# Kernel tuning notes

Hardware: AMD Instinct MI355X
Metric: run time of the kernel (lower is better)

Reference implementation:

```python
import jax, jax.numpy as jnp
import numpy as np

B, T, D_IN, EMB, H = 2, 2048, 1024, 1024, 16
HD = EMB // H  # head_dim = 64


def setup_inputs() -> dict:
    key = jax.random.key(0)
    ks = jax.random.split(key, 3)
    scale_qkv = 1.0 / np.sqrt(D_IN)
    scale_o = 1.0 / np.sqrt(EMB)
    return {
        "x": jax.random.normal(ks[0], (B, T, D_IN), dtype=jnp.float32),
        "W_qkv": jax.random.normal(ks[1], (D_IN, 3 * EMB), dtype=jnp.float32) * scale_qkv,
        "b_qkv": jnp.zeros((3 * EMB,), dtype=jnp.float32),
        "W_o": jax.random.normal(ks[2], (EMB, EMB), dtype=jnp.float32) * scale_o,
        "b_o": jnp.zeros((EMB,), dtype=jnp.float32),
    }


def reference(x, W_qkv, b_qkv, W_o, b_o):
    b, t, _ = x.shape
    qkv = x @ W_qkv + b_qkv                      # [B,T,3*EMB]
    # Match torch: reshape to (B,T,H,3*HD) -> permute -> chunk into q,k,v
    qkv = qkv.reshape(b, t, H, 3 * HD).transpose(0, 2, 1, 3)  # [B,H,T,3*HD]
    q, k, v = jnp.split(qkv, 3, axis=-1)         # each [B,H,T,HD]
    scale = 1.0 / jnp.sqrt(jnp.asarray(HD, dtype=q.dtype))
    scores = jnp.einsum("bhqd,bhkd->bhqk", q, k) * scale  # [B,H,T,T]
    attn = jax.nn.softmax(scores, axis=-1)
    values = jnp.einsum("bhqk,bhkd->bhqd", attn, v)       # [B,H,T,HD]
    values = values.transpose(0, 2, 1, 3).reshape(b, t, EMB)
    return values @ W_o + b_o
```

## Files before the change

kernel.cpp:

```cpp
#include <hip/hip_runtime.h>
#include <math.h>

typedef __bf16 bf16x8 __attribute__((ext_vector_type(8)));
typedef float f32x4 __attribute__((ext_vector_type(4)));

#define GPTR(p) ((const __attribute__((address_space(1))) void*)(p))
#define LPTR(p) ((__attribute__((address_space(3))) void*)(p))

#define QSCALE 0.18033688011112042f

__device__ __forceinline__ unsigned short f2bf(float f) {
  unsigned int u = __float_as_uint(f);
  u += 0x7FFFu + ((u >> 16) & 1u);
  return (unsigned short)(u >> 16);
}

__device__ __forceinline__ unsigned int pack_bf2(float lo, float hi) {
  return __builtin_amdgcn_perm(__float_as_uint(hi) + 0x8000u,
                               __float_as_uint(lo) + 0x8000u, 0x07060302u);
}

__device__ __forceinline__ float fast_exp2(float x) {
#if __has_builtin(__builtin_amdgcn_exp2f)
  return __builtin_amdgcn_exp2f(x);
#else
  return exp2f(x);
#endif
}

__device__ __forceinline__ f32x4 zero4() {
  f32x4 z; z[0] = 0.f; z[1] = 0.f; z[2] = 0.f; z[3] = 0.f; return z;
}

__device__ __forceinline__ void permlane_swap32(unsigned int& a, unsigned int& b) {
  asm("v_permlane32_swap_b32 %0, %1" : "+v"(a), "+v"(b));
}
__device__ __forceinline__ void permlane_swap16(unsigned int& a, unsigned int& b) {
  asm("v_permlane16_swap_b32 %0, %1" : "+v"(a), "+v"(b));
}

__global__ void prep(const float* __restrict__ x, unsigned short* __restrict__ xb,
                     const float* __restrict__ Wqkv, unsigned short* __restrict__ wqkvt,
                     const float* __restrict__ Wo, unsigned short* __restrict__ wot) {
  __shared__ float tile[64][65];
  const int bid = blockIdx.x, t = threadIdx.x;
  if (bid < 4096) {
    int i = (bid * 256 + t) * 4;
    float4 v = *(const float4*)(x + i);
    ushort4 o;
    o.x = f2bf(v.x); o.y = f2bf(v.y); o.z = f2bf(v.z); o.w = f2bf(v.w);
    *(ushort4*)(xb + i) = o;
    return;
  }
  const float* in; unsigned short* out; int K, N, bx, by;
  if (bid < 4096 + 768) {
    int id = bid - 4096; bx = id % 48; by = id / 48;
    in = Wqkv; out = wqkvt; K = 1024; N = 3072;
  } else {
    int id = bid - 4864; bx = id % 16; by = id / 16;
    in = Wo; out = wot; K = 1024; N = 1024;
  }
  int k0 = by * 64, n0 = bx * 64;
#pragma unroll
  for (int p = 0; p < 16; ++p) {
    int l = p * 256 + t; int r = l >> 6, c = l & 63;
    tile[r][c] = in[(size_t)(k0 + r) * N + n0 + c];
  }
  __syncthreads();
#pragma unroll
  for (int p = 0; p < 16; ++p) {
    int l = p * 256 + t; int r = l >> 6, c = l & 63;
    out[(size_t)(n0 + r) * K + k0 + c] = f2bf(tile[c][r]);
  }
}

__global__ __launch_bounds__(256) void gemm_qkv(
    const unsigned short* __restrict__ A, const unsigned short* __restrict__ Bt,
    const float* __restrict__ bias,
    unsigned short* __restrict__ Qd, unsigned short* __restrict__ Kd,
    unsigned short* __restrict__ Vtd) {
  __shared__ unsigned short As[2][4096];
  __shared__ unsigned short Bs[2][4096];
  const int tid = threadIdx.x, wave = tid >> 6, lane = tid & 63;
  const int quad = lane >> 4, l16 = lane & 15;
  const int wm = (wave >> 1) * 64, wn = (wave & 1) * 64;
  const int flat = blockIdx.y * 24 + blockIdx.x;
  const int nf = (flat & 7) * 96 + (flat >> 3);
  const int m0 = (nf / 24) * 128, n0 = (nf % 24) * 128;
  f32x4 acc[4][4];
#pragma unroll
  for (int i = 0; i < 4; ++i)
#pragma unroll
    for (int j = 0; j < 4; ++j) acc[i][j] = zero4();

  const int c = wave * 64 + lane;
  const int rA = c >> 2, o16 = (c & 3) * 8;

#define STAGEQ(B, K0)                                                                      \
  do {                                                                                     \
    __builtin_amdgcn_global_load_lds(GPTR(A + (size_t)(m0 + rA) * 1024 + (K0) + o16),      \
                                     LPTR(&As[B][wave * 512]), 16, 0, 0);                  \
    __builtin_amdgcn_global_load_lds(GPTR(A + (size_t)(m0 + 64 + rA) * 1024 + (K0) + o16), \
                                     LPTR(&As[B][2048 + wave * 512]), 16, 0, 0);           \
    __builtin_amdgcn_global_load_lds(GPTR(Bt + (size_t)(n0 + rA) * 1024 + (K0) + o16),     \
                                     LPTR(&Bs[B][wave * 512]), 16, 0, 0);                  \
    __builtin_amdgcn_global_load_lds(GPTR(Bt + (size_t)(n0 + 64 + rA) * 1024 + (K0) + o16),\
                                     LPTR(&Bs[B][2048 + wave * 512]), 16, 0, 0);           \
  } while (0)

  STAGEQ(0, 0);
  __syncthreads();
  int cur = 0;
  for (int k0 = 0; k0 < 1024; k0 += 32) {
    if (k0 < 992) STAGEQ(cur ^ 1, k0 + 32);
    bf16x8 af[4], bfr[4];
#pragma unroll
    for (int mt = 0; mt < 4; ++mt)
      af[mt] = *(const bf16x8*)(&As[cur][(wm + mt * 16 + l16) * 32 + quad * 8]);
#pragma unroll
    for (int nt = 0; nt < 4; ++nt)
      bfr[nt] = *(const bf16x8*)(&Bs[cur][(wn + nt * 16 + l16) * 32 + quad * 8]);
#pragma unroll
    for (int mt = 0; mt < 4; ++mt)
#pragma unroll
      for (int nt = 0; nt < 4; ++nt)
        acc[mt][nt] = __builtin_amdgcn_mfma_f32_16x16x32_bf16(af[mt], bfr[nt], acc[mt][nt], 0, 0, 0);
    __syncthreads();
    cur ^= 1;
  }
#undef STAGEQ

#pragma unroll
  for (int mt = 0; mt < 4; ++mt) {
#pragma unroll
    for (int nt = 0; nt < 4; ++nt) {
      int m = m0 + wm + mt * 16 + quad * 4;
      int n = n0 + wn + nt * 16 + l16;
      float bv = bias[n];
      int h = n / 192, rem = n - h * 192;
      int which = rem >> 6, d = rem & 63;
      int b = m >> 11, t0 = m & 2047;
      size_t head = (size_t)(b * 16 + h);
      f32x4 a = acc[mt][nt];
      if (which == 0) {
        size_t base = (head * 2048 + t0) * 64 + d;
#pragma unroll
        for (int i = 0; i < 4; ++i)
          Qd[base + (size_t)i * 64] = f2bf((a[i] + bv) * QSCALE);
      } else if (which == 1) {
        size_t base = head * 131072 + (size_t)(t0 >> 6) * 4096;
#pragma unroll
        for (int i = 0; i < 4; ++i) {
          int tt = t0 + i;
          Kd[base + (tt & 63) * 64 + (((d >> 3) ^ (tt & 7)) << 3) + (d & 7)] = f2bf(a[i] + bv);
        }
      } else {
        size_t base = head * 131072 + (size_t)(t0 >> 6) * 4096;
        ushort4 o;
        o.x = f2bf(a[0] + bv); o.y = f2bf(a[1] + bv);
        o.z = f2bf(a[2] + bv); o.w = f2bf(a[3] + bv);
        *(ushort4*)(Vtd + base + d * 64 + (((((t0 & 63) >> 3)) ^ (d & 7)) << 3) + (t0 & 7)) = o;
      }
    }
  }
}

__global__ __launch_bounds__(256, 2) void flash_attn(
    const unsigned short* __restrict__ Qg,
    const unsigned short* __restrict__ Kg,
    const unsigned short* __restrict__ Vg,
    unsigned short* __restrict__ att) {
  __shared__ unsigned short SM[16384];
  __shared__ float Lbuf[2][64];
  const int tid = threadIdx.x, wave = tid >> 6, lane = tid & 63;
  const int quad = lane >> 4, l16 = lane & 15;
  const int h7 = l16 & 7;
  const int wq = wave >> 1, wk = wave & 1;
  const int flat = blockIdx.y * 16 + blockIdx.x;
  const int nf = (flat & 7) * 64 + (flat >> 3);
  const int bh = nf >> 4;
  const int q0 = (nf & 15) * 128 + wq * 64;

  bf16x8 bq[4][2];
#pragma unroll
  for (int qg = 0; qg < 4; ++qg)
#pragma unroll
    for (int kh = 0; kh < 2; ++kh)
      bq[qg][kh] = *(const bf16x8*)(Qg + ((size_t)bh * 2048 + q0 + qg * 16 + l16) * 64 + kh * 32 + quad * 8);

  union { unsigned short u[8]; bf16x8 v; } onesu;
#pragma unroll
  for (int i = 0; i < 8; ++i) onesu.u[i] = 0x3F80;
  const bf16x8 ones = onesu.v;

  f32x4 o[4][4], l_acc[4];
#pragma unroll
  for (int qg = 0; qg < 4; ++qg) {
    l_acc[qg] = zero4();
#pragma unroll
    for (int i = 0; i < 4; ++i) o[qg][i] = zero4();
  }

  const unsigned short* Kt = Kg + (size_t)bh * 131072 + lane * 8;
  const unsigned short* Vt = Vg + (size_t)bh * 131072 + lane * 8;
  unsigned short* KsB = SM;
  unsigned short* VsB = SM + 8192;
  const int so0 = wave * 512, so1 = (4 + wave) * 512;

#define STAGE_KV(buf, tile)                                                              \
  do {                                                                                   \
    const unsigned short* Kb_ = Kt + (tile) * 4096;                                      \
    const unsigned short* Vb_ = Vt + (tile) * 4096;                                      \
    __builtin_amdgcn_global_load_lds(GPTR(Kb_ + so0), LPTR(KsB + (buf) * 4096 + so0), 16, 0, 0); \
    __builtin_amdgcn_global_load_lds(GPTR(Kb_ + so1), LPTR(KsB + (buf) * 4096 + so1), 16, 0, 0); \
    __builtin_amdgcn_global_load_lds(GPTR(Vb_ + so0), LPTR(VsB + (buf) * 4096 + so0), 16, 0, 0); \
    __builtin_amdgcn_global_load_lds(GPTR(Vb_ + so1), LPTR(VsB + (buf) * 4096 + so1), 16, 0, 0); \
  } while (0)

  STAGE_KV(0, 0);
  __syncthreads();

  int cur = 0;
  for (int tile = 0; tile < 32; ++tile) {
    if (tile < 31) STAGE_KV(cur ^ 1, tile + 1);
    const unsigned short* Kc = KsB + cur * 4096;
    const unsigned short* Vc = VsB + cur * 4096;

    f32x4 s[4][2];
#pragma unroll
    for (int qg = 0; qg < 4; ++qg) { s[qg][0] = zero4(); s[qg][1] = zero4(); }
#pragma unroll
    for (int kt = 0; kt < 2; ++kt) {
#pragma unroll
      for (int kh = 0; kh < 2; ++kh) {
        bf16x8 a = *(const bf16x8*)(Kc + (wk * 32 + kt * 16 + l16) * 64 + (((kh * 4 + quad) ^ h7) << 3));
#pragma unroll
        for (int qg = 0; qg < 4; ++qg)
          s[qg][kt] = __builtin_amdgcn_mfma_f32_16x16x32_bf16(a, bq[qg][kh], s[qg][kt], 0, 0, 0);
      }
    }

    unsigned int pw[4][2][2];
#pragma unroll
    for (int qg = 0; qg < 4; ++qg) {
#pragma unroll
      for (int kt = 0; kt < 2; ++kt) {
        float p0 = fast_exp2(s[qg][kt][0]);
        float p1 = fast_exp2(s[qg][kt][1]);
        float p2 = fast_exp2(s[qg][kt][2]);
        float p3 = fast_exp2(s[qg][kt][3]);
        pw[qg][kt][0] = pack_bf2(p0, p1);
        pw[qg][kt][1] = pack_bf2(p2, p3);
      }
    }

    bf16x8 pf[4];
#pragma unroll
    for (int qg = 0; qg < 4; ++qg) {
      unsigned int a0 = pw[qg][0][0], b0 = pw[qg][1][0];
      unsigned int a1 = pw[qg][0][1], b1 = pw[qg][1][1];
      permlane_swap32(a0, b0); permlane_swap16(a0, b0);
      permlane_swap32(a1, b1); permlane_swap16(a1, b1);
      union { unsigned int u[4]; bf16x8 v; } x;
      x.u[0] = a0; x.u[1] = a1; x.u[2] = b0; x.u[3] = b1;
      pf[qg] = x.v;
    }

#pragma unroll
    for (int qg = 0; qg < 4; ++qg)
      l_acc[qg] = __builtin_amdgcn_mfma_f32_16x16x32_bf16(ones, pf[qg], l_acc[qg], 0, 0, 0);

#pragma unroll
    for (int mt = 0; mt < 4; ++mt) {
      bf16x8 av = *(const bf16x8*)(Vc + (mt * 16 + l16) * 64 + (((wk * 4 + quad) ^ h7) << 3));
#pragma unroll
      for (int qg = 0; qg < 4; ++qg)
        o[qg][mt] = __builtin_amdgcn_mfma_f32_16x16x32_bf16(av, pf[qg], o[qg][mt], 0, 0, 0);
    }

    __syncthreads();
    cur ^= 1;
  }
#undef STAGE_KV

  float* Obuf = (float*)SM;
  if (wk == 1) {
#pragma unroll
    for (int qg = 0; qg < 4; ++qg) {
#pragma unroll
      for (int mt = 0; mt < 4; ++mt) {
        int cc = (mt * 4 + quad) ^ l16;
        *(f32x4*)(Obuf + wq * 4096 + (qg * 16 + l16) * 64 + cc * 4) = o[qg][mt];
      }
      if (quad == 0) Lbuf[wq][qg * 16 + l16] = l_acc[qg][0];
    }
  }
  __syncthreads();
  if (wk == 0) {
    int b = bh >> 4, h = bh & 15;
#pragma unroll
    for (int qg = 0; qg < 4; ++qg) {
      float inv_l = 1.f / (l_acc[qg][0] + Lbuf[wq][qg * 16 + l16]);
      unsigned short* orow = att + ((size_t)b * 2048 + q0 + qg * 16 + l16) * 1024 + h * 64;
#pragma unroll
      for (int mt = 0; mt < 4; ++mt) {
        int cc = (mt * 4 + quad) ^ l16;
        f32x4 other = *(const f32x4*)(Obuf + wq * 4096 + (qg * 16 + l16) * 64 + cc * 4);
        ushort4 ov;
        ov.x = f2bf((o[qg][mt][0] + other[0]) * inv_l);
        ov.y = f2bf((o[qg][mt][1] + other[1]) * inv_l);
        ov.z = f2bf((o[qg][mt][2] + other[2]) * inv_l);
        ov.w = f2bf((o[qg][mt][3] + other[3]) * inv_l);
        *(ushort4*)(orow + mt * 16 + quad * 4) = ov;
      }
    }
  }
}

__global__ __launch_bounds__(256) void gemm_out(
    const unsigned short* __restrict__ A, const unsigned short* __restrict__ Bt,
    const float* __restrict__ bias, float* __restrict__ out) {
  __shared__ unsigned short As[2][4096];
  __shared__ unsigned short Bs[2][2048];
  const int tid = threadIdx.x, wave = tid >> 6, lane = tid & 63;
  const int quad = lane >> 4, l16 = lane & 15;
  const int wm = (wave >> 1) * 64, wn = (wave & 1) * 32;
  const int flat = blockIdx.y * 16 + blockIdx.x;
  const int nf = (flat & 7) * 64 + (flat >> 3);
  const int m0 = (nf >> 4) * 128, n0 = (nf & 15) * 64;
  f32x4 acc[4][2];
#pragma unroll
  for (int i = 0; i < 4; ++i)
#pragma unroll
    for (int j = 0; j < 2; ++j) acc[i][j] = zero4();

  const int c = wave * 64 + lane;
  const int rA = c >> 2, o16 = (c & 3) * 8;

#define STAGEO(B, K0)                                                                      \
  do {                                                                                     \
    __builtin_amdgcn_global_load_lds(GPTR(A + (size_t)(m0 + rA) * 1024 + (K0) + o16),      \
                                     LPTR(&As[B][wave * 512]), 16, 0, 0);                  \
    __builtin_amdgcn_global_load_lds(GPTR(A + (size_t)(m0 + 64 + rA) * 1024 + (K0) + o16), \
                                     LPTR(&As[B][2048 + wave * 512]), 16, 0, 0);           \
    __builtin_amdgcn_global_load_lds(GPTR(Bt + (size_t)(n0 + rA) * 1024 + (K0) + o16),     \
                                     LPTR(&Bs[B][wave * 512]), 16, 0, 0);                  \
  } while (0)

  STAGEO(0, 0);
  __syncthreads();
  int cur = 0;
  for (int k0 = 0; k0 < 1024; k0 += 32) {
    if (k0 < 992) STAGEO(cur ^ 1, k0 + 32);
    bf16x8 af[4], bfr[2];
#pragma unroll
    for (int mt = 0; mt < 4; ++mt)
      af[mt] = *(const bf16x8*)(&As[cur][(wm + mt * 16 + l16) * 32 + quad * 8]);
#pragma unroll
    for (int nt = 0; nt < 2; ++nt)
      bfr[nt] = *(const bf16x8*)(&Bs[cur][(wn + nt * 16 + l16) * 32 + quad * 8]);
#pragma unroll
    for (int mt = 0; mt < 4; ++mt)
#pragma unroll
      for (int nt = 0; nt < 2; ++nt)
        acc[mt][nt] = __builtin_amdgcn_mfma_f32_16x16x32_bf16(af[mt], bfr[nt], acc[mt][nt], 0, 0, 0);
    __syncthreads();
    cur ^= 1;
  }
#undef STAGEO

#pragma unroll
  for (int mt = 0; mt < 4; ++mt) {
#pragma unroll
    for (int nt = 0; nt < 2; ++nt) {
      int m = m0 + wm + mt * 16 + quad * 4;
      int n = n0 + wn + nt * 16 + l16;
      float bv = bias[n];
      float* orow = out + (size_t)m * 1024 + n;
      orow[0]        = acc[mt][nt][0] + bv;
      orow[1024]     = acc[mt][nt][1] + bv;
      orow[2 * 1024] = acc[mt][nt][2] + bv;
      orow[3 * 1024] = acc[mt][nt][3] + bv;
    }
  }
}

extern "C" void kernel_launch(void* const* d_in, const int* in_sizes, int n_in,
                              void* d_out, int out_size, void* d_ws, size_t ws_size,
                              hipStream_t stream) {
  const float* x    = (const float*)d_in[0];
  const float* Wqkv = (const float*)d_in[1];
  const float* bqkv = (const float*)d_in[2];
  const float* Wo   = (const float*)d_in[3];
  const float* bo   = (const float*)d_in[4];
  float* out = (float*)d_out;

  unsigned short* xb    = (unsigned short*)d_ws;
  unsigned short* wqkvt = xb    + (size_t)4096 * 1024;
  unsigned short* wot   = wqkvt + (size_t)3072 * 1024;
  unsigned short* Qd    = wot   + (size_t)1024 * 1024;
  unsigned short* Kd    = Qd    + (size_t)32 * 2048 * 64;
  unsigned short* Vtd   = Kd    + (size_t)32 * 2048 * 64;
  unsigned short* attb  = Vtd   + (size_t)32 * 2048 * 64;

  prep<<<4096 + 768 + 256, 256, 0, stream>>>(x, xb, Wqkv, wqkvt, Wo, wot);
  gemm_qkv<<<dim3(24, 32), 256, 0, stream>>>(xb, wqkvt, bqkv, Qd, Kd, Vtd);
  flash_attn<<<dim3(16, 32), 256, 0, stream>>>(Qd, Kd, Vtd, attb);
  gemm_out<<<dim3(16, 32), 256, 0, stream>>>(attb, wot, bo, out);
}
```

Before: 190.0 us.

## Split attention KV range in two with atomic fp32 partials and combine kernel

```diff
diff --git a/kernel.cpp b/kernel.cpp
--- a/kernel.cpp
+++ b/kernel.cpp
@@ -39,9 +39,8 @@
   asm("v_permlane16_swap_b32 %0, %1" : "+v"(a), "+v"(b));
 }
 
-__global__ void prep(const float* __restrict__ x, unsigned short* __restrict__ xb,
-                     const float* __restrict__ Wqkv, unsigned short* __restrict__ wqkvt,
-                     const float* __restrict__ Wo, unsigned short* __restrict__ wot) {
+__global__ void prep_a(const float* __restrict__ x, unsigned short* __restrict__ xb,
+                       const float* __restrict__ Wqkv, unsigned short* __restrict__ wqkvt) {
   __shared__ float tile[64][65];
   const int bid = blockIdx.x, t = threadIdx.x;
   if (bid < 4096) {
@@ -52,15 +51,28 @@
     *(ushort4*)(xb + i) = o;
     return;
   }
-  const float* in; unsigned short* out; int K, N, bx, by;
-  if (bid < 4096 + 768) {
-    int id = bid - 4096; bx = id % 48; by = id / 48;
-    in = Wqkv; out = wqkvt; K = 1024; N = 3072;
-  } else {
-    int id = bid - 4864; bx = id % 16; by = id / 16;
-    in = Wo; out = wot; K = 1024; N = 1024;
-  }
+  int id = bid - 4096;
+  int bx = id % 48, by = id / 48;
+  const int K = 1024, N = 3072;
   int k0 = by * 64, n0 = bx * 64;
+#pragma unroll
+  for (int p = 0; p < 16; ++p) {
+    int l = p * 256 + t; int r = l >> 6, c = l & 63;
+    tile[r][c] = Wqkv[(size_t)(k0 + r) * N + n0 + c];
+  }
+  __syncthreads();
+#pragma unroll
+  for (int p = 0; p < 16; ++p) {
+    int l = p * 256 + t; int r = l >> 6, c = l & 63;
+    wqkvt[(size_t)(n0 + r) * K + k0 + c] = f2bf(tile[c][r]);
+  }
+}
+
+__global__ void transpose_conv(const float* __restrict__ in, unsigned short* __restrict__ out,
+                               int K, int N) {
+  __shared__ float tile[64][65];
+  int k0 = blockIdx.y * 64, n0 = blockIdx.x * 64;
+  int t = threadIdx.x;
 #pragma unroll
   for (int p = 0; p < 16; ++p) {
     int l = p * 256 + t; int r = l >> 6, c = l & 63;
@@ -169,7 +181,8 @@
     const unsigned short* __restrict__ Qg,
     const unsigned short* __restrict__ Kg,
     const unsigned short* __restrict__ Vg,
-    unsigned short* __restrict__ att) {
+    float* __restrict__ Po,
+    float* __restrict__ Pl) {
   __shared__ unsigned short SM[16384];
   __shared__ float Lbuf[2][64];
   const int tid = threadIdx.x, wave = tid >> 6, lane = tid & 63;
@@ -177,9 +190,12 @@
   const int h7 = l16 & 7;
   const int wq = wave >> 1, wk = wave & 1;
   const int flat = blockIdx.y * 16 + blockIdx.x;
-  const int nf = (flat & 7) * 64 + (flat >> 3);
-  const int bh = nf >> 4;
-  const int q0 = (nf & 15) * 128 + wq * 64;
+  const int nf = (flat & 7) * 128 + (flat >> 3);
+  const int bh = nf >> 5;
+  const int half = (nf >> 4) & 1;
+  const int qb = nf & 15;
+  const int q0 = qb * 128 + wq * 64;
+  const int tbase = half * 16;
 
   bf16x8 bq[4][2];
 #pragma unroll
@@ -217,12 +233,12 @@
     __builtin_amdgcn_global_load_lds(GPTR(Vb_ + so1), LPTR(VsB + (buf) * 4096 + so1), 16, 0, 0); \
   } while (0)
 
-  STAGE_KV(0, 0);
+  STAGE_KV(0, tbase);
   __syncthreads();
 
   int cur = 0;
-  for (int tile = 0; tile < 32; ++tile) {
-    if (tile < 31) STAGE_KV(cur ^ 1, tile + 1);
+  for (int it = 0; it < 16; ++it) {
+    if (it < 15) STAGE_KV(cur ^ 1, tbase + it + 1);
     const unsigned short* Kc = KsB + cur * 4096;
     const unsigned short* Vc = VsB + cur * 4096;
 
@@ -297,24 +313,40 @@
   }
   __syncthreads();
   if (wk == 0) {
-    int b = bh >> 4, h = bh & 15;
 #pragma unroll
     for (int qg = 0; qg < 4; ++qg) {
-      float inv_l = 1.f / (l_acc[qg][0] + Lbuf[wq][qg * 16 + l16]);
-      unsigned short* orow = att + ((size_t)b * 2048 + q0 + qg * 16 + l16) * 1024 + h * 64;
+      size_t prow = (size_t)bh * 2048 + q0 + qg * 16 + l16;
+      float* po = Po + prow * 64;
+      float lsum = l_acc[qg][0] + Lbuf[wq][qg * 16 + l16];
 #pragma unroll
       for (int mt = 0; mt < 4; ++mt) {
         int cc = (mt * 4 + quad) ^ l16;
         f32x4 other = *(const f32x4*)(Obuf + wq * 4096 + (qg * 16 + l16) * 64 + cc * 4);
-        ushort4 ov;
-        ov.x = f2bf((o[qg][mt][0] + other[0]) * inv_l);
-        ov.y = f2bf((o[qg][mt][1] + other[1]) * inv_l);
-        ov.z = f2bf((o[qg][mt][2] + other[2]) * inv_l);
-        ov.w = f2bf((o[qg][mt][3] + other[3]) * inv_l);
-        *(ushort4*)(orow + mt * 16 + quad * 4) = ov;
+#pragma unroll
+        for (int i = 0; i < 4; ++i)
+          atomicAdd(po + mt * 16 + quad * 4 + i, o[qg][mt][i] + other[i]);
       }
-    }
-  }
+      if (quad == 0) atomicAdd(Pl + prow, lsum);
+    }
+  }
+}
+
+__global__ __launch_bounds__(256) void combine_attn(
+    const float* __restrict__ Po, const float* __restrict__ Pl,
+    unsigned short* __restrict__ att) {
+  int g = blockIdx.x * 256 + threadIdx.x;
+  int row = g >> 4;
+  int dq = (g & 15) * 4;
+  int bh = row >> 11, q = row & 2047;
+  float inv = 1.f / Pl[row];
+  float4 a = *(const float4*)(Po + (size_t)row * 64 + dq);
+  ushort4 o;
+  o.x = f2bf(a.x * inv);
+  o.y = f2bf(a.y * inv);
+  o.z = f2bf(a.z * inv);
+  o.w = f2bf(a.w * inv);
+  int b_ = bh >> 4, h = bh & 15;
+  *(ushort4*)(att + ((size_t)(b_ * 2048 + q)) * 1024 + h * 64 + dq) = o;
 }
 
 __global__ __launch_bounds__(256) void gemm_out(
@@ -398,13 +430,19 @@
   unsigned short* xb    = (unsigned short*)d_ws;
   unsigned short* wqkvt = xb    + (size_t)4096 * 1024;
   unsigned short* wot   = wqkvt + (size_t)3072 * 1024;
+  float*          Po    = (float*)d_ws;
   unsigned short* Qd    = wot   + (size_t)1024 * 1024;
   unsigned short* Kd    = Qd    + (size_t)32 * 2048 * 64;
   unsigned short* Vtd   = Kd    + (size_t)32 * 2048 * 64;
   unsigned short* attb  = Vtd   + (size_t)32 * 2048 * 64;
-
-  prep<<<4096 + 768 + 256, 256, 0, stream>>>(x, xb, Wqkv, wqkvt, Wo, wot);
+  float*          Pl    = out;
+
+  prep_a<<<4096 + 768, 256, 0, stream>>>(x, xb, Wqkv, wqkvt);
   gemm_qkv<<<dim3(24, 32), 256, 0, stream>>>(xb, wqkvt, bqkv, Qd, Kd, Vtd);
-  flash_attn<<<dim3(16, 32), 256, 0, stream>>>(Qd, Kd, Vtd, attb);
+  hipMemsetAsync(Po, 0, (size_t)65536 * 64 * sizeof(float), stream);
+  hipMemsetAsync(Pl, 0, (size_t)65536 * sizeof(float), stream);
+  flash_attn<<<dim3(16, 64), 256, 0, stream>>>(Qd, Kd, Vtd, Po, Pl);
+  combine_attn<<<4096, 256, 0, stream>>>(Po, Pl, attb);
+  transpose_conv<<<dim3(16, 16), 256, 0, stream>>>(Wo, wot, 1024, 1024);
   gemm_out<<<dim3(16, 32), 256, 0, stream>>>(attb, wot, bo, out);
 }
```

Result: slower. 322.0 us (+69.5%).
